# Kernel optimization log

Measured on AMD Instinct MI355X. Metric: run time of the kernel, lower is better.

## Reference

```python
import jax, jax.numpy as jnp
import numpy as np


def setup_inputs() -> dict:
    key = jax.random.key(0)
    k1, k2, k3, k4, k5, k6 = jax.random.split(key, 6)
    B, C, H, W = 8, 128, 256, 256
    Ch = C // 2
    u = jax.random.normal(k1, (B, C, H, W), dtype=jnp.float32)
    weights_input = jax.random.normal(k2, (B, C, H, W), dtype=jnp.float32)
    # 1x1 conv params (stored as [out, in])
    w1 = jax.random.normal(k3, (Ch, C), dtype=jnp.float32) * (1.0 / np.sqrt(C))
    b1 = jax.random.normal(k4, (Ch,), dtype=jnp.float32) * 0.01
    w2 = jax.random.normal(k5, (4, Ch), dtype=jnp.float32) * (1.0 / np.sqrt(Ch))
    b2 = jax.random.normal(k6, (4,), dtype=jnp.float32) * 0.01
    return {"u": u, "weights_input": weights_input, "w1": w1, "b1": b1, "w2": w2, "b2": b2}


def _shift_up(u):  # neighbor above: zero-pad top row
    return jnp.pad(u[:, :, :-1, :], ((0, 0), (0, 0), (1, 0), (0, 0)))


def _shift_down(u):
    return jnp.pad(u[:, :, 1:, :], ((0, 0), (0, 0), (0, 1), (0, 0)))


def _shift_left(u):
    return jnp.pad(u[:, :, :, :-1], ((0, 0), (0, 0), (0, 0), (1, 0)))


def _shift_right(u):
    return jnp.pad(u[:, :, :, 1:], ((0, 0), (0, 0), (0, 0), (0, 1)))


def reference(u, weights_input, w1, b1, w2, b2):
    # weight_net: 1x1 conv -> ReLU -> 1x1 conv -> Softplus
    h = jax.nn.relu(jnp.einsum('bchw,oc->bohw', weights_input, w1) + b1[None, :, None, None])
    w = jax.nn.softplus(jnp.einsum('bchw,oc->bohw', h, w2) + b2[None, :, None, None])  # (B,4,H,W)
    w_up, w_down, w_left, w_right = w[:, 0:1], w[:, 1:2], w[:, 2:3], w[:, 3:4]
    lap = (w_up * (_shift_up(u) - u)
           + w_down * (_shift_down(u) - u)
           + w_left * (_shift_left(u) - u)
           + w_right * (_shift_right(u) - u))
    return lap
```

## Files before the change

### kernel.cpp

```cpp
#include <hip/hip_runtime.h>
#include <math.h>

constexpr int Bn = 8, Cn = 128, ChN = 64, Hn = 256, Wn = 256;
constexpr long long HWn  = (long long)Hn * Wn;
constexpr long long CHWn = (long long)Cn * HWn;

typedef short  s16x8  __attribute__((ext_vector_type(8)));
typedef __bf16 bf16x8 __attribute__((ext_vector_type(8)));
typedef float  f32x4  __attribute__((ext_vector_type(4)));

static __device__ __forceinline__ unsigned short f2bf(float f) {
    union { float f; unsigned u; } v; v.f = f;
    unsigned r = (v.u + 0x7FFFu + ((v.u >> 16) & 1u)) >> 16;
    return (unsigned short)r;
}
static __device__ __forceinline__ bf16x8 tobf(s16x8 s) {
    bf16x8 r; __builtin_memcpy(&r, &s, 16); return r;
}

__global__ void prep(const float* __restrict__ w1, const float* __restrict__ w2,
                     uint4* __restrict__ af, float* __restrict__ w2t) {
    int idx = blockIdx.x * 256 + threadIdx.x;
    if (idx < 1024) {
        int lane = idx & 63, kb = (idx >> 6) & 3, ot = idx >> 8;
        int row   = ot * 16 + (lane & 15);
        int kbase = kb * 32 + ((lane >> 4) & 3) * 8;
        const float* src = w1 + row * Cn + kbase;
        unsigned short b[8];
        #pragma unroll
        for (int t = 0; t < 8; ++t) b[t] = f2bf(src[t]);
        uint4 r;
        r.x = (unsigned)b[0] | ((unsigned)b[1] << 16);
        r.y = (unsigned)b[2] | ((unsigned)b[3] << 16);
        r.z = (unsigned)b[4] | ((unsigned)b[5] << 16);
        r.w = (unsigned)b[6] | ((unsigned)b[7] << 16);
        af[idx] = r;
    } else if (idx < 1024 + ChN * 4) {
        int t = idx - 1024;
        w2t[t] = w2[(t & 3) * ChN + (t >> 2)];
    }
}

__device__ __forceinline__ float softplus_f(float x) {
    return fmaxf(x, 0.0f) + log1pf(expf(-fabsf(x)));
}

__global__ __launch_bounds__(256) void wfield(
    const float* __restrict__ wi,
    const uint4* __restrict__ af,
    const float* __restrict__ w2t,
    const float* __restrict__ b1,
    const float* __restrict__ b2,
    float* __restrict__ wpk)
{
    const int tid  = threadIdx.x;
    const int wv   = tid >> 6;
    const int lane = tid & 63;
    const int l15  = lane & 15;
    const int lg   = lane >> 4;

    const int wid = blockIdx.x * 4 + wv;

    for (int q = 0; q < 2; ++q) {
        const int grp = wid * 2 + q;
        const int p0  = grp * 32;
        const int bb  = p0 >> 16;
        const int rem = p0 & (int)(HWn - 1);

        const float* wip = wi + (size_t)bb * CHWn + rem + 2 * l15;

        float2 xb[32];
        #pragma unroll
        for (int kb = 0; kb < 4; ++kb)
            #pragma unroll
            for (int t = 0; t < 8; ++t)
                xb[kb * 8 + t] = *(const float2*)(wip + (size_t)(kb * 32 + lg * 8 + t) * HWn);

        f32x4 accA[4], accB[4];
        #pragma unroll
        for (int ot = 0; ot < 4; ++ot) {
            f32x4 b1v = *(const f32x4*)(b1 + ot * 16 + lg * 4);
            accA[ot] = b1v;
            accB[ot] = b1v;
        }

        #pragma unroll
        for (int kb = 0; kb < 4; ++kb) {
            s16x8 bsA, bsB;
            #pragma unroll
            for (int t = 0; t < 8; ++t) {
                bsA[t] = (short)f2bf(xb[kb * 8 + t].x);
                bsB[t] = (short)f2bf(xb[kb * 8 + t].y);
            }
            bf16x8 bfA = tobf(bsA), bfB = tobf(bsB);
            #pragma unroll
            for (int ot = 0; ot < 4; ++ot) {
                s16x8 as = ((const s16x8*)af)[(ot * 4 + kb) * 64 + lane];
                bf16x8 av = tobf(as);
                accA[ot] = __builtin_amdgcn_mfma_f32_16x16x32_bf16(av, bfA, accA[ot], 0, 0, 0);
                accB[ot] = __builtin_amdgcn_mfma_f32_16x16x32_bf16(av, bfB, accB[ot], 0, 0, 0);
            }
        }

        float a0A = 0.f, a1A = 0.f, a2A = 0.f, a3A = 0.f;
        float a0B = 0.f, a1B = 0.f, a2B = 0.f, a3B = 0.f;
        #pragma unroll
        for (int ot = 0; ot < 4; ++ot) {
            #pragma unroll
            for (int r = 0; r < 4; ++r) {
                int o = ot * 16 + lg * 4 + r;
                const float4 w4v = ((const float4*)w2t)[o];
                float hA = fmaxf(accA[ot][r], 0.f);
                float hB = fmaxf(accB[ot][r], 0.f);
                a0A = fmaf(w4v.x, hA, a0A); a0B = fmaf(w4v.x, hB, a0B);
                a1A = fmaf(w4v.y, hA, a1A); a1B = fmaf(w4v.y, hB, a1B);
                a2A = fmaf(w4v.z, hA, a2A); a2B = fmaf(w4v.z, hB, a2B);
                a3A = fmaf(w4v.w, hA, a3A); a3B = fmaf(w4v.w, hB, a3B);
            }
        }
        a0A += __shfl_xor(a0A, 16); a0A += __shfl_xor(a0A, 32);
        a1A += __shfl_xor(a1A, 16); a1A += __shfl_xor(a1A, 32);
        a2A += __shfl_xor(a2A, 16); a2A += __shfl_xor(a2A, 32);
        a3A += __shfl_xor(a3A, 16); a3A += __shfl_xor(a3A, 32);
        a0B += __shfl_xor(a0B, 16); a0B += __shfl_xor(a0B, 32);
        a1B += __shfl_xor(a1B, 16); a1B += __shfl_xor(a1B, 32);
        a2B += __shfl_xor(a2B, 16); a2B += __shfl_xor(a2B, 32);
        a3B += __shfl_xor(a3B, 16); a3B += __shfl_xor(a3B, 32);

        if (lg == 0) {
            const int i  = (p0 >> 8) & 255;
            const int jA = (p0 & 255) + 2 * l15;
            float* wrow = wpk + ((size_t)(bb * Hn + i) * 4) * Wn;
            wrow[0 * Wn + jA] = softplus_f(a0A + b2[0]);
            wrow[1 * Wn + jA] = softplus_f(a1A + b2[1]);
            wrow[2 * Wn + jA] = softplus_f(a2A + b2[2]);
            wrow[3 * Wn + jA] = softplus_f(a3A + b2[3]);
            wrow[0 * Wn + jA + 1] = softplus_f(a0B + b2[0]);
            wrow[1 * Wn + jA + 1] = softplus_f(a1B + b2[1]);
            wrow[2 * Wn + jA + 1] = softplus_f(a2B + b2[2]);
            wrow[3 * Wn + jA + 1] = softplus_f(a3B + b2[3]);
        }
    }
}

__global__ __launch_bounds__(256) void stencil5(
    const float* __restrict__ u,
    const float* __restrict__ wpk,
    float* __restrict__ out)
{
    const int bb    = blockIdx.x & 7;
    const int rest  = blockIdx.x >> 3;
    const int strip = rest & 31;
    const int cq    = rest >> 5;
    const int tid   = threadIdx.x;
    const int wv    = tid >> 6;
    const int lane  = tid & 63;

    const int i0 = strip * 8;
    const int c0 = cq * 32 + wv * 8;
    const int j4 = lane * 4;

    __shared__ float wlds[8 * 4 * 256];

    const float* wsrc = wpk + ((size_t)(bb * Hn + i0) * 4) * Wn;
    #pragma unroll
    for (int k = 0; k < 8; ++k) {
        f32x4 v = *(const f32x4*)(wsrc + (size_t)(k * 256 + tid) * 4);
        *(f32x4*)(wlds + (k * 256 + tid) * 4) = v;
    }
    __syncthreads();

    const float4 z4 = {0.f, 0.f, 0.f, 0.f};

    #pragma unroll 2
    for (int cc = 0; cc < 8; ++cc) {
        const int c = c0 + cc;
        const size_t plane = ((size_t)bb * Cn + c) * HWn;
        const float* up0 = u   + plane + j4;
        float*       po  = out + plane + j4;

        float4 R[10];
        #pragma unroll
        for (int k = 0; k < 10; ++k) {
            const int i = i0 - 1 + k;
            R[k] = (i >= 0 && i < Hn) ? *(const float4*)(up0 + (size_t)i * Wn) : z4;
        }

        #pragma unroll
        for (int r = 0; r < 8; ++r) {
            float4 ctr = R[r + 1], up4 = R[r], dn4 = R[r + 2];
            const f32x4* wrow = (const f32x4*)(wlds + (size_t)(r * 4) * 256);
            f32x4 WU = wrow[0 * 64 + lane];
            f32x4 WD = wrow[1 * 64 + lane];
            f32x4 WL = wrow[2 * 64 + lane];
            f32x4 WR = wrow[3 * 64 + lane];

            float lw = __shfl(ctr.w, lane - 1);
            float rw = __shfl(ctr.x, lane + 1);
            float lfx = (lane == 0)  ? 0.f : lw;
            float rtw = (lane == 63) ? 0.f : rw;

            f32x4 WS = (WU + WD) + (WL + WR);

            f32x4 res;
            res[0] = fmaf(WU[0], up4.x, fmaf(WD[0], dn4.x, fmaf(WL[0], lfx,   fmaf(WR[0], ctr.y, -WS[0] * ctr.x))));
            res[1] = fmaf(WU[1], up4.y, fmaf(WD[1], dn4.y, fmaf(WL[1], ctr.x, fmaf(WR[1], ctr.z, -WS[1] * ctr.y))));
            res[2] = fmaf(WU[2], up4.z, fmaf(WD[2], dn4.z, fmaf(WL[2], ctr.y, fmaf(WR[2], ctr.w, -WS[2] * ctr.z))));
            res[3] = fmaf(WU[3], up4.w, fmaf(WD[3], dn4.w, fmaf(WL[3], ctr.z, fmaf(WR[3], rtw,   -WS[3] * ctr.w))));

            *(f32x4*)(po + (size_t)(i0 + r) * Wn) = res;
        }
    }
}

extern "C" void kernel_launch(void* const* d_in, const int* in_sizes, int n_in,
                              void* d_out, int out_size, void* d_ws, size_t ws_size,
                              hipStream_t stream) {
    const float* u  = (const float*)d_in[0];
    const float* wi = (const float*)d_in[1];
    const float* w1 = (const float*)d_in[2];
    const float* b1 = (const float*)d_in[3];
    const float* w2 = (const float*)d_in[4];
    const float* b2 = (const float*)d_in[5];
    float* out = (float*)d_out;

    uint4* af  = (uint4*)d_ws;
    float* w2t = (float*)((char*)d_ws + 16384);
    float* wpk = (float*)((char*)d_ws + 17408);

    prep<<<5, 256, 0, stream>>>(w1, w2, af, w2t);
    wfield<<<2048, 256, 0, stream>>>(wi, af, w2t, b1, b2, wpk);
    stencil5<<<1024, 256, 0, stream>>>(u, wpk, out);
}
```

Measured before the change: 189.8 us.

## Replace strip-tiled stencil with grid-stride row stencil loading weights from global

Replaces the stencil kernel, which staged an 8-row weight tile in LDS and walked 8 channels with register row reuse, with a grid-stride kernel. Each thread handles one float4 per iteration, loads the up/down neighbours and the four weight rows directly from global memory, and relies on cache for reuse. This removes the LDS staging, the block barrier and the register pressure from the 10-row window. In exchange each point re-reads its vertical neighbours and weight rows, which raises L2 traffic, and it changes the grid to 2048 blocks.

```diff
diff --git a/kernel.cpp b/kernel.cpp
--- a/kernel.cpp
+++ b/kernel.cpp
@@ -143,73 +143,47 @@
     }
 }
 
-__global__ __launch_bounds__(256) void stencil5(
+__global__ __launch_bounds__(256) void stencil_gs(
     const float* __restrict__ u,
     const float* __restrict__ wpk,
     float* __restrict__ out)
 {
-    const int bb    = blockIdx.x & 7;
-    const int rest  = blockIdx.x >> 3;
-    const int strip = rest & 31;
-    const int cq    = rest >> 5;
-    const int tid   = threadIdx.x;
-    const int wv    = tid >> 6;
-    const int lane  = tid & 63;
-
-    const int i0 = strip * 8;
-    const int c0 = cq * 32 + wv * 8;
-    const int j4 = lane * 4;
-
-    __shared__ float wlds[8 * 4 * 256];
-
-    const float* wsrc = wpk + ((size_t)(bb * Hn + i0) * 4) * Wn;
-    #pragma unroll
-    for (int k = 0; k < 8; ++k) {
-        f32x4 v = *(const f32x4*)(wsrc + (size_t)(k * 256 + tid) * 4);
-        *(f32x4*)(wlds + (k * 256 + tid) * 4) = v;
-    }
-    __syncthreads();
-
-    const float4 z4 = {0.f, 0.f, 0.f, 0.f};
+    const int tid  = threadIdx.x;
+    const int lane = tid & 63;
+    const size_t base0 = (size_t)blockIdx.x * 256 + tid;
+    const f32x4 z4 = {0.f, 0.f, 0.f, 0.f};
 
     #pragma unroll 2
-    for (int cc = 0; cc < 8; ++cc) {
-        const int c = c0 + cc;
-        const size_t plane = ((size_t)bb * Cn + c) * HWn;
-        const float* up0 = u   + plane + j4;
-        float*       po  = out + plane + j4;
-
-        float4 R[10];
-        #pragma unroll
-        for (int k = 0; k < 10; ++k) {
-            const int i = i0 - 1 + k;
-            R[k] = (i >= 0 && i < Hn) ? *(const float4*)(up0 + (size_t)i * Wn) : z4;
-        }
-
-        #pragma unroll
-        for (int r = 0; r < 8; ++r) {
-            float4 ctr = R[r + 1], up4 = R[r], dn4 = R[r + 2];
-            const f32x4* wrow = (const f32x4*)(wlds + (size_t)(r * 4) * 256);
-            f32x4 WU = wrow[0 * 64 + lane];
-            f32x4 WD = wrow[1 * 64 + lane];
-            f32x4 WL = wrow[2 * 64 + lane];
-            f32x4 WR = wrow[3 * 64 + lane];
-
-            float lw = __shfl(ctr.w, lane - 1);
-            float rw = __shfl(ctr.x, lane + 1);
-            float lfx = (lane == 0)  ? 0.f : lw;
-            float rtw = (lane == 63) ? 0.f : rw;
-
-            f32x4 WS = (WU + WD) + (WL + WR);
-
-            f32x4 res;
-            res[0] = fmaf(WU[0], up4.x, fmaf(WD[0], dn4.x, fmaf(WL[0], lfx,   fmaf(WR[0], ctr.y, -WS[0] * ctr.x))));
-            res[1] = fmaf(WU[1], up4.y, fmaf(WD[1], dn4.y, fmaf(WL[1], ctr.x, fmaf(WR[1], ctr.z, -WS[1] * ctr.y))));
-            res[2] = fmaf(WU[2], up4.z, fmaf(WD[2], dn4.z, fmaf(WL[2], ctr.y, fmaf(WR[2], ctr.w, -WS[2] * ctr.z))));
-            res[3] = fmaf(WU[3], up4.w, fmaf(WD[3], dn4.w, fmaf(WL[3], ctr.z, fmaf(WR[3], rtw,   -WS[3] * ctr.w))));
-
-            *(f32x4*)(po + (size_t)(i0 + r) * Wn) = res;
-        }
+    for (int it = 0; it < 32; ++it) {
+        const size_t g = base0 + (size_t)it * (2048 * 256);
+        const int i = (int)((g >> 6) & 255);
+        const int b = (int)(g >> 21);
+
+        const float* cp = u + g * 4;
+        f32x4 ctr = *(const f32x4*)cp;
+        f32x4 up4 = (i > 0)       ? *(const f32x4*)(cp - Wn) : z4;
+        f32x4 dn4 = (i < Hn - 1)  ? *(const f32x4*)(cp + Wn) : z4;
+
+        const float* wrow = wpk + (((size_t)(b * Hn + i) * 4) << 8) + 4 * lane;
+        f32x4 WU = *(const f32x4*)(wrow + 0 * Wn);
+        f32x4 WD = *(const f32x4*)(wrow + 1 * Wn);
+        f32x4 WL = *(const f32x4*)(wrow + 2 * Wn);
+        f32x4 WR = *(const f32x4*)(wrow + 3 * Wn);
+
+        float lw = __shfl(ctr[3], lane - 1);
+        float rw = __shfl(ctr[0], lane + 1);
+        float lfx = (lane == 0)  ? 0.f : lw;
+        float rtw = (lane == 63) ? 0.f : rw;
+
+        f32x4 WS = (WU + WD) + (WL + WR);
+
+        f32x4 res;
+        res[0] = fmaf(WU[0], up4[0], fmaf(WD[0], dn4[0], fmaf(WL[0], lfx,    fmaf(WR[0], ctr[1], -WS[0] * ctr[0]))));
+        res[1] = fmaf(WU[1], up4[1], fmaf(WD[1], dn4[1], fmaf(WL[1], ctr[0], fmaf(WR[1], ctr[2], -WS[1] * ctr[1]))));
+        res[2] = fmaf(WU[2], up4[2], fmaf(WD[2], dn4[2], fmaf(WL[2], ctr[1], fmaf(WR[2], ctr[3], -WS[2] * ctr[2]))));
+        res[3] = fmaf(WU[3], up4[3], fmaf(WD[3], dn4[3], fmaf(WL[3], ctr[2], fmaf(WR[3], rtw,    -WS[3] * ctr[3]))));
+
+        *(f32x4*)(out + g * 4) = res;
     }
 }
 
@@ -230,5 +204,5 @@
 
     prep<<<5, 256, 0, stream>>>(w1, w2, af, w2t);
     wfield<<<2048, 256, 0, stream>>>(wi, af, w2t, b1, b2, wpk);
-    stencil5<<<1024, 256, 0, stream>>>(u, wpk, out);
-}
+    stencil_gs<<<2048, 256, 0, stream>>>(u, wpk, out);
+}
```

Result: slower. 255.4 us (+34.6%).
